# Kernel optimization log

Hardware: AMD Instinct MI355X
Metric: run time of the kernel (lower is better)

## Reference

```python
import jax, jax.numpy as jnp
import numpy as np

HIDDEN = 896
N_HEADS = 14
N_KV_HEADS = 2
HEAD_DIM = HIDDEN // N_HEADS  # 64
KV_GROUPS = N_HEADS // N_KV_HEADS  # 7
ROPE_THETA = 1000000.0


def rotate_half(x):
    x1, x2 = x[..., : x.shape[-1] // 2], x[..., x.shape[-1] // 2 :]
    return jnp.concatenate((-x2, x1), axis=-1)


def rope_tables(seq_len, dtype=jnp.float32):
    inv_freq = 1.0 / (ROPE_THETA ** (jnp.arange(0, HEAD_DIM, 2, dtype=jnp.float32) / HEAD_DIM))
    t = jnp.arange(seq_len, dtype=jnp.float32)
    freqs = jnp.outer(t, inv_freq)            # [S, D/2]
    emb = jnp.concatenate((freqs, freqs), -1)  # [S, D]
    return jnp.cos(emb).astype(dtype), jnp.sin(emb).astype(dtype)


def setup_inputs() -> dict:
    key = jax.random.key(0)
    ks = jax.random.split(key, 8)
    B, S = 2, 2048
    s = 0.02
    return {
        "hidden_states": jax.random.normal(ks[0], (B, S, HIDDEN), jnp.float32),
        "wq": jax.random.normal(ks[1], (HIDDEN, N_HEADS * HEAD_DIM), jnp.float32) * s,
        "bq": jnp.zeros((N_HEADS * HEAD_DIM,), jnp.float32),
        "wk": jax.random.normal(ks[2], (HIDDEN, N_KV_HEADS * HEAD_DIM), jnp.float32) * s,
        "bk": jnp.zeros((N_KV_HEADS * HEAD_DIM,), jnp.float32),
        "wv": jax.random.normal(ks[3], (HIDDEN, N_KV_HEADS * HEAD_DIM), jnp.float32) * s,
        "bv": jnp.zeros((N_KV_HEADS * HEAD_DIM,), jnp.float32),
        "wo": jax.random.normal(ks[4], (N_HEADS * HEAD_DIM, HIDDEN), jnp.float32) * s,
    }


def reference(hidden_states, wq, bq, wk, bk, wv, bv, wo):
    B, S, _ = hidden_states.shape
    q = (hidden_states @ wq + bq).reshape(B, S, N_HEADS, HEAD_DIM)
    k = (hidden_states @ wk + bk).reshape(B, S, N_KV_HEADS, HEAD_DIM)
    v = (hidden_states @ wv + bv).reshape(B, S, N_KV_HEADS, HEAD_DIM)

    cos, sin = rope_tables(S, hidden_states.dtype)
    cos, sin = cos[None, :, None, :], sin[None, :, None, :]
    q = q * cos + rotate_half(q) * sin
    k = k * cos + rotate_half(k) * sin

    # GQA broadcast: repeat kv heads to match query heads
    k = jnp.repeat(k, KV_GROUPS, axis=2)
    v = jnp.repeat(v, KV_GROUPS, axis=2)

    # [B, H, S, S]
    scores = jnp.einsum("bqhd,bkhd->bhqk", q, k) / jnp.sqrt(jnp.asarray(HEAD_DIM, hidden_states.dtype))
    mask = jnp.tril(jnp.ones((S, S), dtype=jnp.bool_))
    scores = jnp.where(mask[None, None, :, :], scores, jnp.asarray(-1e9, scores.dtype))
    attn = jax.nn.softmax(scores, axis=-1)
    out = jnp.einsum("bhqk,bkhd->bqhd", attn, v).reshape(B, S, N_HEADS * HEAD_DIM)
    return out @ wo
```

## Files before the change

kernel.cpp:

```cpp
#include <hip/hip_runtime.h>

#define HID 896
#define NQ 896
#define NKV 128
#define NQKV 1152
#define NH 14
#define NKVH 2
#define GQ 7
#define DH 64
#define SEQ 2048
#define BATCH 2
#define TOK (BATCH*SEQ)

typedef __attribute__((ext_vector_type(8))) short short8;
typedef __attribute__((ext_vector_type(4))) float f32x4;
typedef __attribute__((ext_vector_type(4))) unsigned short us4;

__device__ __forceinline__ unsigned short f2bf(float x) {
  unsigned int u = __builtin_bit_cast(unsigned int, x);
  u = (u + 0x7fffu + ((u >> 16) & 1u)) >> 16;
  return (unsigned short)u;
}
__device__ __forceinline__ float bf2f(unsigned short b) {
  return __builtin_bit_cast(float, (unsigned int)b << 16);
}
__device__ __forceinline__ f32x4 fzero4() {
  f32x4 z; z[0]=0.f; z[1]=0.f; z[2]=0.f; z[3]=0.f; return z;
}
__device__ __forceinline__ unsigned int cvt_pk_bf16(float lo, float hi) {
  unsigned int r;
  asm("v_cvt_pk_bf16_f32 %0, %1, %2" : "=v"(r) : "v"(lo), "v"(hi));
  return r;
}
__device__ __forceinline__ void gload_lds16(const unsigned short* g, unsigned short* l) {
  __builtin_amdgcn_global_load_lds(
      (const __attribute__((address_space(1))) void*)(const void*)g,
      (__attribute__((address_space(3))) void*)(void*)l, 16, 0, 0);
}

#define CVT_BLKS 3584
#define TRN_BLKS 448
#define BIAS_BLKS 5
#define TAB_BLKS 256
#define PREP_BLKS (CVT_BLKS + TRN_BLKS + BIAS_BLKS + TAB_BLKS)

__global__ void k_prep(const float* __restrict__ hs,
                       const float* __restrict__ wq, const float* __restrict__ bq,
                       const float* __restrict__ wk, const float* __restrict__ bk,
                       const float* __restrict__ wv, const float* __restrict__ bv,
                       const float* __restrict__ wo,
                       unsigned short* __restrict__ hb,
                       unsigned short* __restrict__ wqkvt,
                       unsigned short* __restrict__ wot,
                       float* __restrict__ bqkv,
                       float2* __restrict__ cs) {
  __shared__ unsigned short Ls[64*65];
  int blk = blockIdx.x, tid = threadIdx.x;
  if (blk < CVT_BLKS) {
    int i = blk*256 + tid;
    float4 v = ((const float4*)hs)[i];
    us4 o; o[0]=f2bf(v.x); o[1]=f2bf(v.y); o[2]=f2bf(v.z); o[3]=f2bf(v.w);
    ((us4*)hb)[i] = o;
    return;
  }
  blk -= CVT_BLKS;
  if (blk < TRN_BLKS) {
    const float* W; unsigned short* out; int K, N, n0, k0;
    if (blk < 196)      { W=wq; out=wqkvt;                        K=HID; N=NQ;  int t=blk;     n0=(t%14)*64; k0=(t/14)*64; }
    else if (blk < 224) { W=wk; out=wqkvt + (size_t)NQ*HID;       K=HID; N=NKV; int t=blk-196; n0=(t%2)*64;  k0=(t/2)*64; }
    else if (blk < 252) { W=wv; out=wqkvt + (size_t)(NQ+NKV)*HID; K=HID; N=NKV; int t=blk-224; n0=(t%2)*64;  k0=(t/2)*64; }
    else                { W=wo; out=wot;                          K=NQ;  N=HID; int t=blk-252; n0=(t%14)*64; k0=(t/14)*64; }
    #pragma unroll
    for (int i = 0; i < 16; ++i) {
      int idx = i*256 + tid;
      int r = idx >> 6, c = idx & 63;
      Ls[c*65 + r] = f2bf(W[(size_t)(k0 + r)*N + n0 + c]);
    }
    __syncthreads();
    #pragma unroll
    for (int i = 0; i < 16; ++i) {
      int idx = i*256 + tid;
      int r2 = idx >> 6, c2 = idx & 63;
      out[(size_t)(n0 + r2)*K + k0 + c2] = Ls[r2*65 + c2];
    }
    return;
  }
  blk -= TRN_BLKS;
  if (blk < BIAS_BLKS) {
    int i = blk*256 + tid;
    if (i < NQKV) {
      if (i < NQ) bqkv[i] = bq[i];
      else if (i < NQ + NKV) bqkv[i] = bk[i - NQ];
      else bqkv[i] = bv[i - NQ - NKV];
    }
    return;
  }
  blk -= BIAS_BLKS;
  {
    int i = blk*256 + tid;
    int s = i >> 5, dp = i & 31;
    float inv = __expf(-(float)(2*dp) * (13.815510557964274f / 64.0f));
    float f = (float)s * inv;
    cs[i] = make_float2(cosf(f), sinf(f));
  }
}

template<int OUTMODE>
__global__ __launch_bounds__(256, 3) void k_gemm_bt(
    const unsigned short* __restrict__ A,
    const unsigned short* __restrict__ Bt,
    const float* __restrict__ bias,
    const float2* __restrict__ cs,
    void* __restrict__ Cout,
    unsigned short* __restrict__ Qr,
    unsigned short* __restrict__ Kr,
    unsigned short* __restrict__ Vt,
    int M, int N, int K) {
  __shared__ unsigned short As[2][64*64];
  __shared__ unsigned short Bs[2][128*64];
  int tid = threadIdx.x;
  int lane = tid & 63, w = tid >> 6;
  int wr = w >> 1, wc = w & 1;
  int l15 = lane & 15, l4 = lane >> 4;
  int m0 = blockIdx.y * 64, n0 = blockIdx.x * 128;

  f32x4 acc[2][4];
  #pragma unroll
  for (int i = 0; i < 2; ++i)
    #pragma unroll
    for (int j = 0; j < 4; ++j) acc[i][j] = fzero4();

  auto stage = [&](int kt, int bsel) {
    int k0 = kt << 6;
    #pragma unroll
    for (int t = 0; t < 2; ++t) {
      int chunk = t*256 + w*64 + lane;
      int row = chunk >> 3, sp = chunk & 7;
      int sl = sp ^ (row & 7);
      gload_lds16(A + (size_t)(m0+row)*K + k0 + sl*8, &As[bsel][(t*256 + w*64)*8]);
    }
    #pragma unroll
    for (int t = 0; t < 4; ++t) {
      int chunk = t*256 + w*64 + lane;
      int row = chunk >> 3, sp = chunk & 7;
      int sl = sp ^ (row & 7);
      gload_lds16(Bt + (size_t)(n0+row)*K + k0 + sl*8, &Bs[bsel][(t*256 + w*64)*8]);
    }
  };

  int nkt = K >> 6;
  stage(0, 0);
  __syncthreads();
  int cur = 0;
  for (int kt = 0; kt < nkt; ++kt) {
    if (kt + 1 < nkt) stage(kt + 1, cur ^ 1);
    #pragma unroll
    for (int s = 0; s < 2; ++s) {
      short8 af[2], bfr[4];
      #pragma unroll
      for (int mi = 0; mi < 2; ++mi) {
        int row = wr*32 + mi*16 + l15;
        int slot = (s*4 + l4) ^ (row & 7);
        af[mi] = *reinterpret_cast<const short8*>(&As[cur][row*64 + slot*8]);
      }
      #pragma unroll
      for (int ni = 0; ni < 4; ++ni) {
        int row = wc*64 + ni*16 + l15;
        int slot = (s*4 + l4) ^ (row & 7);
        bfr[ni] = *reinterpret_cast<const short8*>(&Bs[cur][row*64 + slot*8]);
      }
      #pragma unroll
      for (int mi = 0; mi < 2; ++mi)
        #pragma unroll
        for (int ni = 0; ni < 4; ++ni)
          acc[mi][ni] = __builtin_amdgcn_mfma_f32_16x16x32_bf16(af[mi], bfr[ni], acc[mi][ni], 0, 0, 0);
    }
    __syncthreads();
    cur ^= 1;
  }

  if (OUTMODE == 1) {
    #pragma unroll
    for (int mi = 0; mi < 2; ++mi)
      #pragma unroll
      for (int ni = 0; ni < 4; ++ni)
        #pragma unroll
        for (int r = 0; r < 4; ++r) {
          int row = m0 + wr*32 + mi*16 + l4*4 + r;
          int col = n0 + wc*64 + ni*16 + l15;
          ((float*)Cout)[(size_t)row*N + col] = acc[mi][ni][r];
        }
    return;
  }

  int col0 = n0 + wc*64;
  if (col0 < NQ + NKV) {
    #pragma unroll
    for (int mi = 0; mi < 2; ++mi) {
      #pragma unroll
      for (int r = 0; r < 4; ++r) {
        int row = m0 + wr*32 + mi*16 + l4*4 + r;
        int b = row >> 11, s = row & 2047;
        #pragma unroll
        for (int ni = 0; ni < 2; ++ni) {
          int dp = ni*16 + l15;
          float x1 = acc[mi][ni][r]   + bias[col0 + dp];
          float x2 = acc[mi][ni+2][r] + bias[col0 + dp + 32];
          float2 c2 = cs[s*32 + dp];
          if (col0 < NQ) {
            int h = col0 >> 6;
            size_t base = ((size_t)(b*NH + h)*SEQ + s)*64;
            Qr[base + dp]      = f2bf((x1*c2.x - x2*c2.y) * 0.125f);
            Qr[base + dp + 32] = f2bf((x2*c2.x + x1*c2.y) * 0.125f);
          } else {
            int kvh = (col0 - NQ) >> 6;
            size_t base = ((size_t)(b*NKVH + kvh)*SEQ + s)*64;
            Kr[base + dp]      = f2bf(x1*c2.x - x2*c2.y);
            Kr[base + dp + 32] = f2bf(x2*c2.x + x1*c2.y);
          }
        }
      }
    }
  } else {
    int kvh = (col0 - 1024) >> 6;
    unsigned short* scr = &Bs[0][0] + w * (64*40);
    #pragma unroll
    for (int mi = 0; mi < 2; ++mi) {
      #pragma unroll
      for (int ni = 0; ni < 2; ++ni) {
        #pragma unroll
        for (int h2 = 0; h2 < 2; ++h2) {
          int dp = ni*16 + l15 + h2*32;
          float b0 = bias[col0 + dp];
          f32x4 a = acc[mi][ni + h2*2];
          uint2 pk;
          pk.x = cvt_pk_bf16(a[0] + b0, a[1] + b0);
          pk.y = cvt_pk_bf16(a[2] + b0, a[3] + b0);
          *reinterpret_cast<uint2*>(&scr[dp*40 + mi*16 + l4*4]) = pk;
        }
      }
    }
    __syncthreads();
    int srow0 = m0 + wr*32;
    int b = srow0 >> 11, s0 = srow0 & 2047;
    size_t vbase = (size_t)(b*NKVH + kvh)*64;
    #pragma unroll
    for (int p2 = 0; p2 < 4; ++p2) {
      int dp = p2*16 + (lane >> 2);
      int tok0 = (lane & 3) * 8;
      short8 v = *reinterpret_cast<const short8*>(&scr[dp*40 + tok0]);
      *reinterpret_cast<short8*>(&Vt[(vbase + dp)*SEQ + s0 + tok0]) = v;
    }
  }
}

__global__ __launch_bounds__(512, 2) void k_attn(
    const unsigned short* __restrict__ Q,
    const unsigned short* __restrict__ Kr,
    const unsigned short* __restrict__ Vt,
    unsigned short* __restrict__ Aout) {
  __shared__ __align__(16) unsigned short Kst[2][2][64*64];
  __shared__ __align__(16) unsigned short Vst[2][2][64*64];
  __shared__ __align__(16) unsigned short P_lds[8][16*64];
  int lane = threadIdx.x & 63, w = threadIdx.x >> 6;
  int grp = w >> 2, wsub = w & 3;
  int l15 = lane & 15, l4 = lane >> 4;
  int i = blockIdx.x, h = blockIdx.y, b = blockIdx.z;
  int qtH = 31 - i, qtL = i;
  int qt = grp ? qtL : qtH;
  int kvh = h / GQ;
  const unsigned short* Kb = Kr + ((size_t)(b*NKVH + kvh))*SEQ*64;
  const unsigned short* Vb = Vt + ((size_t)(b*NKVH + kvh))*64*SEQ;
  char* Pw = (char*)&P_lds[w][0];

  auto stage = [&](int slab, int bsel) {
    #pragma unroll
    for (int t = 0; t < 2; ++t) {
      int ks = slab*2 + t; if (ks > 31) ks = 31;
      int chunk = w*64 + lane;
      int row = chunk >> 3;
      int sl = (chunk & 7) ^ (row & 7);
      gload_lds16(Kb + (size_t)(ks*64 + row)*64 + sl*8, &Kst[bsel][t][chunk*8]);
      gload_lds16(Vb + (size_t)row*SEQ + ks*64 + sl*8, &Vst[bsel][t][chunk*8]);
    }
  };

  const unsigned short* Qb = Q + (((size_t)(b*NH + h))*SEQ + qt*64 + wsub*16) * 64;
  short8 qa[2];
  #pragma unroll
  for (int s = 0; s < 2; ++s)
    qa[s] = *reinterpret_cast<const short8*>(Qb + l15*64 + s*32 + l4*8);

  f32x4 acc[4];
  #pragma unroll
  for (int n = 0; n < 4; ++n) acc[n] = fzero4();
  float m_run = -__builtin_inff(), l_run = 0.0f;

  stage(0, 0);
  __syncthreads();
  int cur = 0;
  int nkt = qtH + 1;
  int nslab = (nkt + 1) >> 1;

  for (int s = 0; s < nslab; ++s) {
    if (s + 1 < nslab) stage(s + 1, cur ^ 1);
    int ks0 = s*2;
    if (ks0 <= qt) {
      f32x4 sa[2][4];
      #pragma unroll
      for (int t = 0; t < 2; ++t) {
        int ks = ks0 + t;
        if (ks <= qt) {
          const unsigned short* Ks = &Kst[cur][t][0];
          #pragma unroll
          for (int n = 0; n < 4; ++n) sa[t][n] = fzero4();
          __builtin_amdgcn_s_setprio(1);
          #pragma unroll
          for (int si = 0; si < 2; ++si) {
            short8 kb[4];
            #pragma unroll
            for (int n = 0; n < 4; ++n) {
              int row = n*16 + l15;
              int slot = (si*4 + l4) ^ (row & 7);
              kb[n] = *reinterpret_cast<const short8*>(&Ks[row*64 + slot*8]);
            }
            #pragma unroll
            for (int n = 0; n < 4; ++n)
              sa[t][n] = __builtin_amdgcn_mfma_f32_16x16x32_bf16(kb[n], qa[si], sa[t][n], 0, 0, 0);
          }
          __builtin_amdgcn_s_setprio(0);
          if (ks == qt) {
            int q_glob = qt*64 + wsub*16 + l15;
            #pragma unroll
            for (int n = 0; n < 4; ++n)
              #pragma unroll
              for (int r = 0; r < 4; ++r) {
                int kpos = ks*64 + n*16 + l4*4 + r;
                if (kpos > q_glob) sa[t][n][r] = -1e30f;
              }
          }
        } else {
          #pragma unroll
          for (int n = 0; n < 4; ++n)
            #pragma unroll
            for (int r = 0; r < 4; ++r) sa[t][n][r] = -1e30f;
        }
      }
      float tm[2];
      #pragma unroll
      for (int t = 0; t < 2; ++t) {
        float t0 = fmaxf(fmaxf(sa[t][0][0],sa[t][0][1]), fmaxf(sa[t][0][2],sa[t][0][3]));
        float t1 = fmaxf(fmaxf(sa[t][1][0],sa[t][1][1]), fmaxf(sa[t][1][2],sa[t][1][3]));
        float t2 = fmaxf(fmaxf(sa[t][2][0],sa[t][2][1]), fmaxf(sa[t][2][2],sa[t][2][3]));
        float t3 = fmaxf(fmaxf(sa[t][3][0],sa[t][3][1]), fmaxf(sa[t][3][2],sa[t][3][3]));
        tm[t] = fmaxf(fmaxf(t0,t1), fmaxf(t2,t3));
      }
      float tmax = fmaxf(tm[0], tm[1]);
      tmax = fmaxf(tmax, __shfl_xor(tmax, 16));
      tmax = fmaxf(tmax, __shfl_xor(tmax, 32));
      float mn = fmaxf(m_run, tmax);
      float sc = __expf(m_run - mn);
      float sum = 0.0f;
      #pragma unroll
      for (int t = 0; t < 2; ++t) {
        #pragma unroll
        for (int n = 0; n < 4; ++n)
          #pragma unroll
          for (int r = 0; r < 4; ++r) sa[t][n][r] = __expf(sa[t][n][r] - mn);
        float s0 = (sa[t][0][0]+sa[t][0][1]) + (sa[t][0][2]+sa[t][0][3]);
        float s1 = (sa[t][1][0]+sa[t][1][1]) + (sa[t][1][2]+sa[t][1][3]);
        float s2 = (sa[t][2][0]+sa[t][2][1]) + (sa[t][2][2]+sa[t][2][3]);
        float s3 = (sa[t][3][0]+sa[t][3][1]) + (sa[t][3][2]+sa[t][3][3]);
        sum += (s0+s1) + (s2+s3);
      }
      m_run = mn;
      l_run = l_run*sc + sum;
      #pragma unroll
      for (int n = 0; n < 4; ++n) acc[n] *= sc;
      #pragma unroll
      for (int t = 0; t < 2; ++t) {
        if (ks0 + t <= qt) {
          #pragma unroll
          for (int n = 0; n < 4; ++n) {
            uint2 pk;
            pk.x = cvt_pk_bf16(sa[t][n][0], sa[t][n][1]);
            pk.y = cvt_pk_bf16(sa[t][n][2], sa[t][n][3]);
            int colbyte = n*32 + l4*8;
            int addr = l15*128 + ((((colbyte>>4) ^ (l15&7))) << 4) + (colbyte & 15);
            *reinterpret_cast<uint2*>(Pw + addr) = pk;
          }
          const unsigned short* Vs = &Vst[cur][t][0];
          __builtin_amdgcn_s_setprio(1);
          #pragma unroll
          for (int s2i = 0; s2i < 2; ++s2i) {
            int pslot = (s2i*4 + l4) ^ (l15 & 7);
            short8 pa = *reinterpret_cast<const short8*>(Pw + l15*128 + pslot*16);
            #pragma unroll
            for (int n = 0; n < 4; ++n) {
              int row = n*16 + l15;
              int vslot = (s2i*4 + l4) ^ (row & 7);
              short8 vb = *reinterpret_cast<const short8*>(&Vs[row*64 + vslot*8]);
              acc[n] = __builtin_amdgcn_mfma_f32_16x16x32_bf16(vb, pa, acc[n], 0, 0, 0);
            }
          }
          __builtin_amdgcn_s_setprio(0);
        }
      }
    }
    __syncthreads();
    cur ^= 1;
  }

  float lt = l_run;
  lt += __shfl_xor(lt, 16);
  lt += __shfl_xor(lt, 32);
  float inv = 1.0f / lt;
  #pragma unroll
  for (int n = 0; n < 4; ++n) {
    uint2 pk;
    pk.x = cvt_pk_bf16(acc[n][0]*inv, acc[n][1]*inv);
    pk.y = cvt_pk_bf16(acc[n][2]*inv, acc[n][3]*inv);
    int colbyte = n*32 + l4*8;
    int addr = l15*128 + ((((colbyte>>4) ^ (l15&7))) << 4) + (colbyte & 15);
    *reinterpret_cast<uint2*>(Pw + addr) = pk;
  }
  int row = lane >> 2;
  int cb0 = (lane & 3) * 32;
  #pragma unroll
  for (int it = 0; it < 2; ++it) {
    int cb = cb0 + it*16;
    int slot = (cb >> 4) ^ (row & 7);
    short8 v = *reinterpret_cast<const short8*>(Pw + row*128 + slot*16);
    size_t tok = (size_t)b*SEQ + qt*64 + wsub*16 + row;
    *reinterpret_cast<short8*>(&Aout[tok*NQ + h*64 + (cb>>1)]) = v;
  }
}

extern "C" void kernel_launch(void* const* d_in, const int* in_sizes, int n_in,
                              void* d_out, int out_size, void* d_ws, size_t ws_size,
                              hipStream_t stream) {
  const float* hs = (const float*)d_in[0];
  const float* wq = (const float*)d_in[1];
  const float* bq = (const float*)d_in[2];
  const float* wk = (const float*)d_in[3];
  const float* bk = (const float*)d_in[4];
  const float* wv = (const float*)d_in[5];
  const float* bv = (const float*)d_in[6];
  const float* wo = (const float*)d_in[7];
  float* out = (float*)d_out;

  char* p = (char*)d_ws;
  auto alloc = [&](size_t bytes) { char* r = p; p += (bytes + 255) & ~(size_t)255; return r; };
  unsigned short* hb    = (unsigned short*)alloc((size_t)TOK*HID*2);
  unsigned short* wqkvt = (unsigned short*)alloc((size_t)NQKV*HID*2);
  unsigned short* wot   = (unsigned short*)alloc((size_t)HID*NQ*2);
  float*          bqkv  = (float*)alloc(NQKV*4);
  float2*         cs    = (float2*)alloc((size_t)SEQ*32*8);
  unsigned short* q_r   = (unsigned short*)alloc((size_t)BATCH*NH*SEQ*DH*2);
  unsigned short* k_r   = (unsigned short*)alloc((size_t)BATCH*NKVH*SEQ*DH*2);
  unsigned short* v_t   = (unsigned short*)alloc((size_t)BATCH*NKVH*DH*SEQ*2);
  unsigned short* attn  = (unsigned short*)alloc((size_t)TOK*NQ*2);

  k_prep<<<PREP_BLKS, 256, 0, stream>>>(hs, wq, bq, wk, bk, wv, bv, wo,
                                        hb, wqkvt, wot, bqkv, cs);
  k_gemm_bt<0><<<dim3(NQKV/128, TOK/64), 256, 0, stream>>>(
      hb, wqkvt, bqkv, cs, nullptr, q_r, k_r, v_t, TOK, NQKV, HID);
  k_attn<<<dim3(16, NH, BATCH), 512, 0, stream>>>(q_r, k_r, v_t, attn);
  k_gemm_bt<1><<<dim3(NQ/128, TOK/64), 256, 0, stream>>>(
      attn, wot, nullptr, nullptr, out, nullptr, nullptr, nullptr, TOK, NQ, HID);
}
```

Before: 86.99 us.

## Fuse fp32-to-bf16 hidden-state conversion into QKV GEMM A-tile loading

Removes the separate bf16 conversion pass over hidden_states from the prep kernel. The QKV projection GEMM now reads fp32 activations directly into registers, converts them to bf16 with packed conversion instructions, and writes them into the swizzled LDS tile after the MFMA work of the current step. This drops a full write and reread of the bf16 activation buffer. In exchange, A loads use register staging instead of async global-to-LDS copies, which raises register pressure and reads 2x the bytes per tile, and each of the 9 N-blocks re-reads the fp32 rows.

```diff
diff --git a/kernel.cpp b/kernel.cpp
--- a/kernel.cpp
+++ b/kernel.cpp
@@ -38,32 +38,21 @@
       (__attribute__((address_space(3))) void*)(void*)l, 16, 0, 0);
 }
 
-#define CVT_BLKS 3584
 #define TRN_BLKS 448
 #define BIAS_BLKS 5
 #define TAB_BLKS 256
-#define PREP_BLKS (CVT_BLKS + TRN_BLKS + BIAS_BLKS + TAB_BLKS)
-
-__global__ void k_prep(const float* __restrict__ hs,
-                       const float* __restrict__ wq, const float* __restrict__ bq,
+#define PREP_BLKS (TRN_BLKS + BIAS_BLKS + TAB_BLKS)
+
+__global__ void k_prep(const float* __restrict__ wq, const float* __restrict__ bq,
                        const float* __restrict__ wk, const float* __restrict__ bk,
                        const float* __restrict__ wv, const float* __restrict__ bv,
                        const float* __restrict__ wo,
-                       unsigned short* __restrict__ hb,
                        unsigned short* __restrict__ wqkvt,
                        unsigned short* __restrict__ wot,
                        float* __restrict__ bqkv,
                        float2* __restrict__ cs) {
   __shared__ unsigned short Ls[64*65];
   int blk = blockIdx.x, tid = threadIdx.x;
-  if (blk < CVT_BLKS) {
-    int i = blk*256 + tid;
-    float4 v = ((const float4*)hs)[i];
-    us4 o; o[0]=f2bf(v.x); o[1]=f2bf(v.y); o[2]=f2bf(v.z); o[3]=f2bf(v.w);
-    ((us4*)hb)[i] = o;
-    return;
-  }
-  blk -= CVT_BLKS;
   if (blk < TRN_BLKS) {
     const float* W; unsigned short* out; int K, N, n0, k0;
     if (blk < 196)      { W=wq; out=wqkvt;                        K=HID; N=NQ;  int t=blk;     n0=(t%14)*64; k0=(t/14)*64; }
@@ -107,7 +96,7 @@
 
 template<int OUTMODE>
 __global__ __launch_bounds__(256, 3) void k_gemm_bt(
-    const unsigned short* __restrict__ A,
+    const void* __restrict__ Ain,
     const unsigned short* __restrict__ Bt,
     const float* __restrict__ bias,
     const float2* __restrict__ cs,
@@ -123,6 +112,8 @@
   int wr = w >> 1, wc = w & 1;
   int l15 = lane & 15, l4 = lane >> 4;
   int m0 = blockIdx.y * 64, n0 = blockIdx.x * 128;
+  const float* Afp = (const float*)Ain;
+  const unsigned short* Ab = (const unsigned short*)Ain;
 
   f32x4 acc[2][4];
   #pragma unroll
@@ -130,15 +121,44 @@
     #pragma unroll
     for (int j = 0; j < 4; ++j) acc[i][j] = fzero4();
 
-  auto stage = [&](int kt, int bsel) {
+  float4 areg[2][2];
+
+  auto loadA = [&](int kt) {
+    int k0 = kt << 6;
+    #pragma unroll
+    for (int c = 0; c < 2; ++c) {
+      int chunk = c*256 + tid;
+      int row = chunk >> 3, sp = chunk & 7;
+      int sl = sp ^ (row & 7);
+      const float* src = Afp + (size_t)(m0+row)*K + k0 + sl*8;
+      areg[c][0] = *reinterpret_cast<const float4*>(src);
+      areg[c][1] = *reinterpret_cast<const float4*>(src + 4);
+    }
+  };
+  auto writeA = [&](int bsel) {
+    #pragma unroll
+    for (int c = 0; c < 2; ++c) {
+      int chunk = c*256 + tid;
+      uint4 pk;
+      pk.x = cvt_pk_bf16(areg[c][0].x, areg[c][0].y);
+      pk.y = cvt_pk_bf16(areg[c][0].z, areg[c][0].w);
+      pk.z = cvt_pk_bf16(areg[c][1].x, areg[c][1].y);
+      pk.w = cvt_pk_bf16(areg[c][1].z, areg[c][1].w);
+      *reinterpret_cast<uint4*>(&As[bsel][chunk*8]) = pk;
+    }
+  };
+  auto stageA16 = [&](int kt, int bsel) {
     int k0 = kt << 6;
     #pragma unroll
     for (int t = 0; t < 2; ++t) {
       int chunk = t*256 + w*64 + lane;
       int row = chunk >> 3, sp = chunk & 7;
       int sl = sp ^ (row & 7);
-      gload_lds16(A + (size_t)(m0+row)*K + k0 + sl*8, &As[bsel][(t*256 + w*64)*8]);
-    }
+      gload_lds16(Ab + (size_t)(m0+row)*K + k0 + sl*8, &As[bsel][(t*256 + w*64)*8]);
+    }
+  };
+  auto stageB = [&](int kt, int bsel) {
+    int k0 = kt << 6;
     #pragma unroll
     for (int t = 0; t < 4; ++t) {
       int chunk = t*256 + w*64 + lane;
@@ -149,11 +169,15 @@
   };
 
   int nkt = K >> 6;
-  stage(0, 0);
+  if (OUTMODE == 0) { loadA(0); writeA(0); } else { stageA16(0, 0); }
+  stageB(0, 0);
   __syncthreads();
   int cur = 0;
   for (int kt = 0; kt < nkt; ++kt) {
-    if (kt + 1 < nkt) stage(kt + 1, cur ^ 1);
+    if (kt + 1 < nkt) {
+      if (OUTMODE == 0) loadA(kt + 1); else stageA16(kt + 1, cur ^ 1);
+      stageB(kt + 1, cur ^ 1);
+    }
     #pragma unroll
     for (int s = 0; s < 2; ++s) {
       short8 af[2], bfr[4];
@@ -175,6 +199,7 @@
         for (int ni = 0; ni < 4; ++ni)
           acc[mi][ni] = __builtin_amdgcn_mfma_f32_16x16x32_bf16(af[mi], bfr[ni], acc[mi][ni], 0, 0, 0);
     }
+    if (OUTMODE == 0 && kt + 1 < nkt) writeA(cur ^ 1);
     __syncthreads();
     cur ^= 1;
   }
@@ -451,7 +476,6 @@
 
   char* p = (char*)d_ws;
   auto alloc = [&](size_t bytes) { char* r = p; p += (bytes + 255) & ~(size_t)255; return r; };
-  unsigned short* hb    = (unsigned short*)alloc((size_t)TOK*HID*2);
   unsigned short* wqkvt = (unsigned short*)alloc((size_t)NQKV*HID*2);
   unsigned short* wot   = (unsigned short*)alloc((size_t)HID*NQ*2);
   float*          bqkv  = (float*)alloc(NQKV*4);
@@ -461,10 +485,10 @@
   unsigned short* v_t   = (unsigned short*)alloc((size_t)BATCH*NKVH*DH*SEQ*2);
   unsigned short* attn  = (unsigned short*)alloc((size_t)TOK*NQ*2);
 
-  k_prep<<<PREP_BLKS, 256, 0, stream>>>(hs, wq, bq, wk, bk, wv, bv, wo,
-                                        hb, wqkvt, wot, bqkv, cs);
+  k_prep<<<PREP_BLKS, 256, 0, stream>>>(wq, bq, wk, bk, wv, bv, wo,
+                                        wqkvt, wot, bqkv, cs);
   k_gemm_bt<0><<<dim3(NQKV/128, TOK/64), 256, 0, stream>>>(
-      hb, wqkvt, bqkv, cs, nullptr, q_r, k_r, v_t, TOK, NQKV, HID);
+      hs, wqkvt, bqkv, cs, nullptr, q_r, k_r, v_t, TOK, NQKV, HID);
   k_attn<<<dim3(16, NH, BATCH), 512, 0, stream>>>(q_r, k_r, v_t, attn);
   k_gemm_bt<1><<<dim3(NQ/128, TOK/64), 256, 0, stream>>>(
       attn, wot, nullptr, nullptr, out, nullptr, nullptr, nullptr, TOK, NQ, HID);
```

Result: slower. 94.92 us (+9.1%).
